# Kernel tuning notes

Hardware: AMD Instinct MI355X
Metric: run time of the kernel (lower is better)

The kernel has to match this reference:

```python
import jax, jax.numpy as jnp
import numpy as np

N_NODES = 100000
N_EDGES = 600000
HID = 128
CH_OUT = 3


def setup_inputs() -> dict:
    key = jax.random.key(0)
    ks = jax.random.split(key, 16)
    s = 0.05  # small init to keep tanh in its linear-ish range
    inp = {
        "x": jax.random.normal(ks[0], (N_NODES, HID), dtype=jnp.float32),
        "pos": jax.random.normal(ks[1], (N_NODES, 3), dtype=jnp.float32),
        "edge_index": jax.random.randint(ks[2], (2, N_EDGES), 0, N_NODES, dtype=jnp.int32),
        "fe_w1": jax.random.normal(ks[3], (2 * HID + 1, HID), dtype=jnp.float32) * s,
        "fe_b1": jnp.zeros((HID,), jnp.float32),
        "fe_w2": jax.random.normal(ks[4], (HID, HID), dtype=jnp.float32) * s,
        "fe_b2": jnp.zeros((HID,), jnp.float32),
        "finf_w": jax.random.normal(ks[5], (HID, 1), dtype=jnp.float32) * s,
        "finf_b": jnp.zeros((1,), jnp.float32),
        "fh_w1": jax.random.normal(ks[6], (2 * HID, HID), dtype=jnp.float32) * s,
        "fh_b1": jnp.zeros((HID,), jnp.float32),
        "fh_w2": jax.random.normal(ks[7], (HID, HID), dtype=jnp.float32) * s,
        "fh_b2": jnp.zeros((HID,), jnp.float32),
        "l1_w": jax.random.normal(ks[8], (HID, HID), dtype=jnp.float32) * s,
        "l1_b": jnp.zeros((HID,), jnp.float32),
        "l2_w": jax.random.normal(ks[9], (HID, HID), dtype=jnp.float32) * s,
        "l2_b": jnp.zeros((HID,), jnp.float32),
        "l3_w": jax.random.normal(ks[10], (HID, HID), dtype=jnp.float32) * s,
        "l3_b": jnp.zeros((HID,), jnp.float32),
        "l4_w": jax.random.normal(ks[11], (HID, HID), dtype=jnp.float32) * s,
        "l4_b": jnp.zeros((HID,), jnp.float32),
        "l5_w": jax.random.normal(ks[12], (HID, CH_OUT), dtype=jnp.float32) * s,
        "l5_b": jnp.zeros((CH_OUT,), jnp.float32),
    }
    return inp


def reference(x, pos, edge_index, fe_w1, fe_b1, fe_w2, fe_b2, finf_w, finf_b,
              fh_w1, fh_b1, fh_w2, fh_b2, l1_w, l1_b, l2_w, l2_b, l3_w, l3_b,
              l4_w, l4_b, l5_w, l5_b):
    e_st, e_end = edge_index[0], edge_index[1]
    # dists = ||(pos_i - pos_j)^2||_2  (norm of the squared difference, as in source)
    d = pos[e_st] - pos[e_end]                                  # [E, 3]
    dists = jnp.linalg.norm(jnp.square(d), axis=1, keepdims=True)  # [E, 1]
    # edge MLP f_e
    tmp = jnp.concatenate([x[e_st], x[e_end], dists], axis=1)   # [E, 2H+1]
    m_ij = jnp.tanh(tmp @ fe_w1 + fe_b1)
    m_ij = jnp.tanh(m_ij @ fe_w2 + fe_b2)                        # [E, H]
    # gating f_inf
    e_ij = jnp.tanh(m_ij @ finf_w + finf_b)                      # [E, 1]
    # scatter-sum to source nodes (index_add on edge_index[0])
    m_i = jax.ops.segment_sum(e_ij * m_ij, e_st, num_segments=x.shape[0])  # [N, H]
    # node update f_h with residual
    h = jnp.concatenate([x, m_i], axis=1)                        # [N, 2H]
    x = x + (jnp.tanh(h @ fh_w1 + fh_b1) @ fh_w2 + fh_b2)
    # dense head (dropout p=0.0 is identity)
    lrelu = lambda v: jax.nn.leaky_relu(v, negative_slope=0.01)
    x = lrelu(x @ l1_w + l1_b)
    x = lrelu(x @ l2_w + l2_b)
    x = lrelu(x @ l3_w + l3_b)
    x = lrelu(x @ l4_w + l4_b)
    return x @ l5_w + l5_b
```

## Files before the change

### kernel.cpp

```cpp
#include <hip/hip_runtime.h>
#include <hip/hip_bf16.h>
#include <math.h>

#define HID 128

typedef unsigned short u16;
typedef __attribute__((ext_vector_type(8))) short bfrag;
typedef __attribute__((ext_vector_type(4))) float f32x4;
typedef __attribute__((ext_vector_type(8))) unsigned short u16x8;
typedef __attribute__((ext_vector_type(4))) unsigned short u16x4;

__device__ __forceinline__ float fast_tanh(float v) {
    float e = __expf(2.0f * v);
    float r = __builtin_amdgcn_rcpf(e + 1.0f);
    return 1.0f - 2.0f * r;
}

__device__ __forceinline__ u16 f2b(float f) {
    __hip_bfloat16 h = __float2bfloat16(f);
    return *(u16*)&h;
}
__device__ __forceinline__ float bits2f(unsigned u) {
    union { unsigned u; float f; } v; v.u = u; return v.f;
}

__global__ void __launch_bounds__(256) prep_combo(
    const float* __restrict__ x, u16* __restrict__ xb,
    const float* __restrict__ w1, const float* __restrict__ fh1,
    const float* __restrict__ w2, const float* __restrict__ fh2,
    const float* __restrict__ l1, const float* __restrict__ l2,
    const float* __restrict__ l3, const float* __restrict__ l4,
    u16* __restrict__ w1t, u16* __restrict__ fh1t,
    u16* __restrict__ w2t, u16* __restrict__ fh2t,
    u16* __restrict__ l1t, u16* __restrict__ l2t,
    u16* __restrict__ l3t, u16* __restrict__ l4t,
    const int* __restrict__ est, int* __restrict__ cnt, int E, int nxb)
{
    int b = blockIdx.x, t = threadIdx.x;
    if (b < nxb) {
        int i = b * 256 + t;
        const float4 v0 = *(const float4*)(x + (size_t)i * 8);
        const float4 v1 = *(const float4*)(x + (size_t)i * 8 + 4);
        u16x8 o = { f2b(v0.x), f2b(v0.y), f2b(v0.z), f2b(v0.w),
                    f2b(v1.x), f2b(v1.y), f2b(v1.z), f2b(v1.w) };
        *(u16x8*)(xb + (size_t)i * 8) = o;
        return;
    }
    b -= nxb;
    if (b < 640) {
        const float* src; u16* dst; int K;
        if (b < 256) {
            K = 256;
            if (b < 128) { src = w1;  dst = w1t; }
            else         { src = fh1; dst = fh1t; b -= 128; }
        } else {
            K = 128;
            int s = (b - 256) >> 6; b = (b - 256) & 63;
            switch (s) {
                case 0:  src = w2;  dst = w2t;  break;
                case 1:  src = fh2; dst = fh2t; break;
                case 2:  src = l1;  dst = l1t;  break;
                case 3:  src = l2;  dst = l2t;  break;
                case 4:  src = l3;  dst = l3t;  break;
                default: src = l4;  dst = l4t;  break;
            }
        }
        int idx = b * 256 + t;
        int k = idx >> 7, n = idx & 127;
        dst[(size_t)n * K + k] = f2b(src[(size_t)k * 128 + n]);
        return;
    }
    b -= 640;
    int e = b * 256 + t;
    if (e < E) atomicAdd(&cnt[est[e]], 1);
}

__global__ void __launch_bounds__(256) scan1(const int* __restrict__ cnt,
                                             int* __restrict__ scanout,
                                             int* __restrict__ partial, int N) {
    __shared__ int s[256];
    int t = threadIdx.x, b = blockIdx.x, i = b * 256 + t;
    int v = (i < N) ? cnt[i] : 0;
    s[t] = v; __syncthreads();
#pragma unroll
    for (int d = 1; d < 256; d <<= 1) {
        int add = (t >= d) ? s[t - d] : 0;
        __syncthreads();
        s[t] += add;
        __syncthreads();
    }
    if (i < N) scanout[i] = s[t] - v;
    if (t == 255) partial[b] = s[255];
}

__global__ void __launch_bounds__(512) scan2(int* __restrict__ partial, int NB) {
    __shared__ int s[512];
    int t = threadIdx.x;
    int v = (t < NB) ? partial[t] : 0;
    s[t] = v; __syncthreads();
#pragma unroll
    for (int d = 1; d < 512; d <<= 1) {
        int add = (t >= d) ? s[t - d] : 0;
        __syncthreads();
        s[t] += add;
        __syncthreads();
    }
    if (t < NB) partial[t] = s[t] - v;
}

__global__ void __launch_bounds__(256) scan3(const int* __restrict__ scanout,
                                             const int* __restrict__ partial,
                                             int* __restrict__ offs,
                                             int* __restrict__ cur, int N, int E) {
    int t = threadIdx.x, b = blockIdx.x, i = b * 256 + t;
    if (i < N) { int o = scanout[i] + partial[b]; offs[i] = o; cur[i] = o; }
    if (i == 0) offs[N] = E;
}

__global__ void __launch_bounds__(256) reorder_kernel(const int* __restrict__ est,
                                                      const int* __restrict__ eend,
                                                      int* __restrict__ cur,
                                                      int* __restrict__ est_s,
                                                      int* __restrict__ eend_s, int E) {
    int e = blockIdx.x * 256 + threadIdx.x;
    if (e < E) {
        int s = est[e];
        int p = atomicAdd(&cur[s], 1);
        est_s[p]  = s;
        eend_s[p] = eend[e];
    }
}

template<int KD>
__device__ __forceinline__ void gemm_k(const u16* sbuf, const u16* __restrict__ wt,
                                       int w, int l16, int l4g, f32x4 (&acc)[2][2]) {
    const int RS = KD * 2;
#pragma unroll
    for (int k0 = 0; k0 < KD; k0 += 32) {
        const int kb = k0 * 2 + l4g * 16;
        bfrag a0 = *(const bfrag*)((const char*)sbuf +
                    (unsigned)((l16 * RS + kb) ^ ((l16 & 7) << 4)));
        bfrag a1 = *(const bfrag*)((const char*)sbuf +
                    (unsigned)(((16 + l16) * RS + kb) ^ ((l16 & 7) << 4)));
        bfrag b0 = *(const bfrag*)((const char*)wt + (size_t)(32 * w + l16) * RS + kb);
        bfrag b1 = *(const bfrag*)((const char*)wt + (size_t)(32 * w + 16 + l16) * RS + kb);
        acc[0][0] = __builtin_amdgcn_mfma_f32_16x16x32_bf16(a0, b0, acc[0][0], 0, 0, 0);
        acc[0][1] = __builtin_amdgcn_mfma_f32_16x16x32_bf16(a0, b1, acc[0][1], 0, 0, 0);
        acc[1][0] = __builtin_amdgcn_mfma_f32_16x16x32_bf16(a1, b0, acc[1][0], 0, 0, 0);
        acc[1][1] = __builtin_amdgcn_mfma_f32_16x16x32_bf16(a1, b1, acc[1][1], 0, 0, 0);
    }
}

template<int KD>
__device__ __forceinline__ void gemm_sw(const u16* act, const u16* __restrict__ wt,
                                        int w, int l16, int l4g, f32x4 (&acc)[2][2]) {
    const int RS = KD * 2;
#pragma unroll
    for (int k0 = 0; k0 < KD; k0 += 32) {
        const int kb = k0 * 2 + l4g * 16;
        bfrag wa0 = *(const bfrag*)((const char*)wt + (size_t)(32 * w + l16) * RS + kb);
        bfrag wa1 = *(const bfrag*)((const char*)wt + (size_t)(32 * w + 16 + l16) * RS + kb);
        bfrag be0 = *(const bfrag*)((const char*)act +
                    (unsigned)((l16 * RS + kb) ^ ((l16 & 7) << 4)));
        bfrag be1 = *(const bfrag*)((const char*)act +
                    (unsigned)(((16 + l16) * RS + kb) ^ ((l16 & 7) << 4)));
        acc[0][0] = __builtin_amdgcn_mfma_f32_16x16x32_bf16(wa0, be0, acc[0][0], 0, 0, 0);
        acc[0][1] = __builtin_amdgcn_mfma_f32_16x16x32_bf16(wa0, be1, acc[0][1], 0, 0, 0);
        acc[1][0] = __builtin_amdgcn_mfma_f32_16x16x32_bf16(wa1, be0, acc[1][0], 0, 0, 0);
        acc[1][1] = __builtin_amdgcn_mfma_f32_16x16x32_bf16(wa1, be1, acc[1][1], 0, 0, 0);
    }
}

__global__ void __launch_bounds__(256, 2)
egc_edge_csr(const u16* __restrict__ xb, const float* __restrict__ pos,
             const int* __restrict__ est_s, const int* __restrict__ eend_s,
             const u16* __restrict__ w1t, const float* __restrict__ w1last,
             const float* __restrict__ b1, const u16* __restrict__ w2t,
             const float* __restrict__ b2, const float* __restrict__ fw,
             const float* __restrict__ fb, u16* __restrict__ g,
             float* __restrict__ ev, int n_tiles)
{
    __shared__ __attribute__((aligned(16))) u16 a_sh[2][32 * 256];
    __shared__ __attribute__((aligned(16))) u16 m1_sh[32 * 128];
    __shared__ float red[32][17];
    __shared__ float dist_l[2][32];

    const int t = threadIdx.x, lane = t & 63, w = t >> 6;
    const int l16 = lane & 15, l4g = lane >> 4;
    const unsigned swz = (unsigned)((l16 & 7) << 4);

    bfrag wa10[8], wa11[8], w2f0[4], w2f1[4];
#pragma unroll
    for (int i = 0; i < 8; ++i) {
        int kb = i * 64 + l4g * 16;
        wa10[i] = *(const bfrag*)((const char*)w1t + (size_t)(32 * w + l16) * 512 + kb);
        wa11[i] = *(const bfrag*)((const char*)w1t + (size_t)(32 * w + 16 + l16) * 512 + kb);
    }
#pragma unroll
    for (int i = 0; i < 4; ++i) {
        int kb = i * 64 + l4g * 16;
        w2f0[i] = *(const bfrag*)((const char*)w2t + (size_t)(32 * w + l16) * 256 + kb);
        w2f1[i] = *(const bfrag*)((const char*)w2t + (size_t)(32 * w + 16 + l16) * 256 + kb);
    }
    float w1l_r[2][4], b1_r[2][4], b2_r[2][4], fw_r[2][4];
#pragma unroll
    for (int mi = 0; mi < 2; ++mi)
#pragma unroll
        for (int rg = 0; rg < 4; ++rg) {
            int n = 32 * w + 16 * mi + l4g * 4 + rg;
            w1l_r[mi][rg] = w1last[n];
            b1_r[mi][rg]  = b1[n];
            b2_r[mi][rg]  = b2[n];
            fw_r[mi][rg]  = fw[n];
        }
    const float fbv = fb[0];

    float4 sv0, sv1, sv2, sv3;
    float pax = 0, pay = 0, paz = 0, pbx = 0, pby = 0, pbz = 0;

#define EDGE_ISSUE(TILE) do {                                                  \
        int e0_ = (TILE) * 32;                                                 \
        { int f_ = t;       int e_ = f_ >> 5, q_ = f_ & 31; int ge_ = e0_ + e_;\
          int nd_ = (q_ < 16) ? est_s[ge_] : eend_s[ge_];                      \
          sv0 = *(const float4*)(xb + (size_t)nd_ * 128 + (q_ & 15) * 8); }    \
        { int f_ = t + 256; int e_ = f_ >> 5, q_ = f_ & 31; int ge_ = e0_ + e_;\
          int nd_ = (q_ < 16) ? est_s[ge_] : eend_s[ge_];                      \
          sv1 = *(const float4*)(xb + (size_t)nd_ * 128 + (q_ & 15) * 8); }    \
        { int f_ = t + 512; int e_ = f_ >> 5, q_ = f_ & 31; int ge_ = e0_ + e_;\
          int nd_ = (q_ < 16) ? est_s[ge_] : eend_s[ge_];                      \
          sv2 = *(const float4*)(xb + (size_t)nd_ * 128 + (q_ & 15) * 8); }    \
        { int f_ = t + 768; int e_ = f_ >> 5, q_ = f_ & 31; int ge_ = e0_ + e_;\
          int nd_ = (q_ < 16) ? est_s[ge_] : eend_s[ge_];                      \
          sv3 = *(const float4*)(xb + (size_t)nd_ * 128 + (q_ & 15) * 8); }    \
        if (t < 32) {                                                          \
            int ge_ = e0_ + t;                                                 \
            int a_ = est_s[ge_], b_ = eend_s[ge_];                             \
            pax = pos[a_ * 3]; pay = pos[a_ * 3 + 1]; paz = pos[a_ * 3 + 2];   \
            pbx = pos[b_ * 3]; pby = pos[b_ * 3 + 1]; pbz = pos[b_ * 3 + 2];   \
        }                                                                      \
    } while (0)

#define EDGE_COMMIT(BUF) do {                                                  \
        { int f_ = t;       int e_ = f_ >> 5, q_ = f_ & 31;                    \
          unsigned by_ = (unsigned)(e_ * 512 + q_ * 16) ^ (unsigned)((e_ & 7) << 4); \
          *(float4*)((char*)a_sh[BUF] + by_) = sv0; }                          \
        { int f_ = t + 256; int e_ = f_ >> 5, q_ = f_ & 31;                    \
          unsigned by_ = (unsigned)(e_ * 512 + q_ * 16) ^ (unsigned)((e_ & 7) << 4); \
          *(float4*)((char*)a_sh[BUF] + by_) = sv1; }                          \
        { int f_ = t + 512; int e_ = f_ >> 5, q_ = f_ & 31;                    \
          unsigned by_ = (unsigned)(e_ * 512 + q_ * 16) ^ (unsigned)((e_ & 7) << 4); \
          *(float4*)((char*)a_sh[BUF] + by_) = sv2; }                          \
        { int f_ = t + 768; int e_ = f_ >> 5, q_ = f_ & 31;                    \
          unsigned by_ = (unsigned)(e_ * 512 + q_ * 16) ^ (unsigned)((e_ & 7) << 4); \
          *(float4*)((char*)a_sh[BUF] + by_) = sv3; }                          \
        if (t < 32) {                                                          \
            float dx_ = pax - pbx, dy_ = pay - pby, dz_ = paz - pbz;           \
            dx_ *= dx_; dy_ *= dy_; dz_ *= dz_;                                \
            dist_l[BUF][t] = sqrtf(dx_ * dx_ + dy_ * dy_ + dz_ * dz_);         \
        }                                                                      \
    } while (0)

    int tile = blockIdx.x;
    EDGE_ISSUE(tile);
    int buf = 0;

    if (tile < n_tiles)
    while (true) {
        EDGE_COMMIT(buf);
        __syncthreads();
        int next = tile + gridDim.x;
        if (next < n_tiles) EDGE_ISSUE(next);
        const int e0 = tile * 32;

        {
            f32x4 acc[2][2] = {};
#pragma unroll
            for (int i = 0; i < 8; ++i) {
                int kb = i * 64 + l4g * 16;
                bfrag be0 = *(const bfrag*)((const char*)a_sh[buf] +
                            ((unsigned)(l16 * 512 + kb) ^ swz));
                bfrag be1 = *(const bfrag*)((const char*)a_sh[buf] +
                            ((unsigned)((16 + l16) * 512 + kb) ^ swz));
                acc[0][0] = __builtin_amdgcn_mfma_f32_16x16x32_bf16(wa10[i], be0, acc[0][0], 0, 0, 0);
                acc[0][1] = __builtin_amdgcn_mfma_f32_16x16x32_bf16(wa10[i], be1, acc[0][1], 0, 0, 0);
                acc[1][0] = __builtin_amdgcn_mfma_f32_16x16x32_bf16(wa11[i], be0, acc[1][0], 0, 0, 0);
                acc[1][1] = __builtin_amdgcn_mfma_f32_16x16x32_bf16(wa11[i], be1, acc[1][1], 0, 0, 0);
            }
            float de0 = dist_l[buf][l16];
            float de1 = dist_l[buf][16 + l16];
#pragma unroll
            for (int mi = 0; mi < 2; ++mi)
#pragma unroll
                for (int ni = 0; ni < 2; ++ni) {
                    float de = ni ? de1 : de0;
                    u16x4 pk;
#pragma unroll
                    for (int rg = 0; rg < 4; ++rg) {
                        float v = fast_tanh(acc[mi][ni][rg] + de * w1l_r[mi][rg] + b1_r[mi][rg]);
                        pk[rg] = f2b(v);
                    }
                    unsigned byte = ((unsigned)((16 * ni + l16) * 256 +
                                     (32 * w + 16 * mi + l4g * 4) * 2)) ^ swz;
                    *(u16x4*)((char*)m1_sh + byte) = pk;
                }
        }
        __syncthreads();

        {
            f32x4 acc[2][2] = {};
#pragma unroll
            for (int i = 0; i < 4; ++i) {
                int kb = i * 64 + l4g * 16;
                bfrag me0 = *(const bfrag*)((const char*)m1_sh +
                            ((unsigned)(l16 * 256 + kb) ^ swz));
                bfrag me1 = *(const bfrag*)((const char*)m1_sh +
                            ((unsigned)((16 + l16) * 256 + kb) ^ swz));
                acc[0][0] = __builtin_amdgcn_mfma_f32_16x16x32_bf16(w2f0[i], me0, acc[0][0], 0, 0, 0);
                acc[0][1] = __builtin_amdgcn_mfma_f32_16x16x32_bf16(w2f0[i], me1, acc[0][1], 0, 0, 0);
                acc[1][0] = __builtin_amdgcn_mfma_f32_16x16x32_bf16(w2f1[i], me0, acc[1][0], 0, 0, 0);
                acc[1][1] = __builtin_amdgcn_mfma_f32_16x16x32_bf16(w2f1[i], me1, acc[1][1], 0, 0, 0);
            }
            float part0 = 0.0f, part1 = 0.0f;
#pragma unroll
            for (int mi = 0; mi < 2; ++mi)
#pragma unroll
                for (int ni = 0; ni < 2; ++ni) {
                    u16x4 pk;
                    float ps = 0.0f;
#pragma unroll
                    for (int rg = 0; rg < 4; ++rg) {
                        float v = fast_tanh(acc[mi][ni][rg] + b2_r[mi][rg]);
                        ps += v * fw_r[mi][rg];
                        pk[rg] = f2b(v);
                    }
                    if (ni) part1 += ps; else part0 += ps;
                    int dstrow = e0 + 16 * ni + l16;
                    *(u16x4*)(g + (size_t)dstrow * 128 + (32 * w + 16 * mi + l4g * 4)) = pk;
                }
            red[l16][w * 4 + l4g]      = part0;
            red[16 + l16][w * 4 + l4g] = part1;
        }
        __syncthreads();

        if (t < 32) {
            float s = 0.0f;
#pragma unroll
            for (int j = 0; j < 16; ++j) s += red[t][j];
            ev[e0 + t] = fast_tanh(s + fbv);
        }

        tile = next; buf ^= 1;
        if (tile >= n_tiles) break;
    }
#undef EDGE_ISSUE
#undef EDGE_COMMIT
}

__global__ void __launch_bounds__(256, 8)
gather_seq(const u16* __restrict__ g, const float* __restrict__ ev,
           const int* __restrict__ offs, u16* __restrict__ m_i)
{
    const int lane = threadIdx.x & 63;
    const int half = lane >> 5;
    const int l32  = lane & 31;
    const int n = blockIdx.x * 4 + (threadIdx.x >> 6);
    const int beg = offs[n], end = offs[n + 1];
    float a0 = 0.0f, a1 = 0.0f, a2 = 0.0f, a3 = 0.0f;
    for (int e = beg + half; e < end; e += 2) {
        uint2 v = *(const uint2*)(g + (size_t)e * 128 + l32 * 4);
        float ee = ev[e];
        a0 += ee * bits2f(v.x << 16);
        a1 += ee * bits2f(v.x & 0xFFFF0000u);
        a2 += ee * bits2f(v.y << 16);
        a3 += ee * bits2f(v.y & 0xFFFF0000u);
    }
    a0 += __shfl_xor(a0, 32);
    a1 += __shfl_xor(a1, 32);
    a2 += __shfl_xor(a2, 32);
    a3 += __shfl_xor(a3, 32);
    if (half == 0) {
        uint2 o;
        o.x = (unsigned)f2b(a0) | ((unsigned)f2b(a1) << 16);
        o.y = (unsigned)f2b(a2) | ((unsigned)f2b(a3) << 16);
        *(uint2*)(m_i + (size_t)n * 128 + l32 * 4) = o;
    }
}

__global__ void __launch_bounds__(256, 3)
egc_edge_mfma(const u16* __restrict__ xb, const float* __restrict__ pos,
              const int* __restrict__ est, const int* __restrict__ eend,
              const u16* __restrict__ w1t, const float* __restrict__ w1last,
              const float* __restrict__ b1, const u16* __restrict__ w2t,
              const float* __restrict__ b2, const float* __restrict__ fw,
              const float* __restrict__ fb, float* __restrict__ m_i)
{
    __shared__ __attribute__((aligned(16))) u16 a_sh[32 * 256];
    __shared__ __attribute__((aligned(16))) u16 m1_sh[32 * 128];
    __shared__ float m2_sh[32][132];
    __shared__ float dist_l[32];
    __shared__ float ev_l[32];
    __shared__ int   st_l[32];

    const int t = threadIdx.x;
    const int e0 = blockIdx.x * 32;
    const int lane = t & 63;
    const int w = t >> 6;
    const int l16 = lane & 15, l4g = lane >> 4;

#pragma unroll
    for (int i = 0; i < 4; ++i) {
        int f = t + 256 * i;
        int e = f >> 5, q = f & 31;
        int ge = e0 + e;
        int node = (q < 16) ? est[ge] : eend[ge];
        float4 v = *(const float4*)(xb + (size_t)node * 128 + (q & 15) * 8);
        unsigned byte = (unsigned)(e * 512 + q * 16) ^ (unsigned)((e & 7) << 4);
        *(float4*)((char*)a_sh + byte) = v;
    }
    if (t < 32) {
        int ge = e0 + t;
        int a = est[ge], b = eend[ge];
        st_l[t] = a;
        float dx = pos[a * 3 + 0] - pos[b * 3 + 0];
        float dy = pos[a * 3 + 1] - pos[b * 3 + 1];
        float dz = pos[a * 3 + 2] - pos[b * 3 + 2];
        dx *= dx; dy *= dy; dz *= dz;
        dist_l[t] = sqrtf(dx * dx + dy * dy + dz * dz);
    }
    __syncthreads();

    {
        f32x4 acc[2][2] = {};
        gemm_k<256>(a_sh, w1t, w, l16, l4g, acc);
#pragma unroll
        for (int mi = 0; mi < 2; ++mi)
#pragma unroll
            for (int ni = 0; ni < 2; ++ni) {
                const int col = 32 * w + 16 * ni + l16;
                const float wl = w1last[col], bb = b1[col];
#pragma unroll
                for (int rg = 0; rg < 4; ++rg) {
                    const int row = 16 * mi + l4g * 4 + rg;
                    float v = fast_tanh(acc[mi][ni][rg] + dist_l[row] * wl + bb);
                    unsigned byte = (unsigned)((row * 256 + col * 2) ^ ((row & 7) << 4));
                    *(u16*)((char*)m1_sh + byte) = f2b(v);
                }
            }
    }
    __syncthreads();

    {
        f32x4 acc[2][2] = {};
        gemm_k<128>(m1_sh, w2t, w, l16, l4g, acc);
#pragma unroll
        for (int mi = 0; mi < 2; ++mi)
#pragma unroll
            for (int ni = 0; ni < 2; ++ni) {
                const int col = 32 * w + 16 * ni + l16;
                const float bb = b2[col];
#pragma unroll
                for (int rg = 0; rg < 4; ++rg) {
                    const int row = 16 * mi + l4g * 4 + rg;
                    m2_sh[row][col] = fast_tanh(acc[mi][ni][rg] + bb);
                }
            }
    }
    __syncthreads();

    if (t < 128) {
        int e = t >> 2, p = t & 3;
        float s = 0.0f;
#pragma unroll
        for (int k = 0; k < 32; ++k) s += m2_sh[e][p * 32 + k] * fw[p * 32 + k];
        s += __shfl_xor(s, 1);
        s += __shfl_xor(s, 2);
        if (p == 0) ev_l[e] = fast_tanh(s + fb[0]);
    }
    __syncthreads();

    {
        int e = t >> 3, l8 = t & 7;
        float ev = ev_l[e];
        size_t base = (size_t)st_l[e] * HID + l8;
#pragma unroll
        for (int i = 0; i < 16; ++i)
            unsafeAtomicAdd(m_i + base + 8 * i, ev * m2_sh[e][l8 + 8 * i]);
    }
}

#define NODE_LAYER_SW(SRC, KD, WT, BIAS, DST, ACT)                             \
    {                                                                          \
        f32x4 acc[2][2] = {};                                                  \
        gemm_sw<KD>(SRC, WT, w, l16, l4g, acc);                                \
        float bbr[2][4];                                                       \
        _Pragma("unroll")                                                      \
        for (int mi = 0; mi < 2; ++mi)                                         \
            _Pragma("unroll")                                                  \
            for (int rg = 0; rg < 4; ++rg)                                     \
                bbr[mi][rg] = (BIAS)[32 * w + 16 * mi + l4g * 4 + rg];         \
        _Pragma("unroll")                                                      \
        for (int mi = 0; mi < 2; ++mi)                                         \
            _Pragma("unroll")                                                  \
            for (int ni = 0; ni < 2; ++ni) {                                   \
                const int node = 16 * ni + l16;                                \
                const int ch = 32 * w + 16 * mi + l4g * 4;                     \
                u16x4 pk;                                                      \
                _Pragma("unroll")                                              \
                for (int rg = 0; rg < 4; ++rg) {                               \
                    float v = acc[mi][ni][rg] + bbr[mi][rg];                   \
                    ACT;                                                       \
                    pk[rg] = f2b(v);                                           \
                }                                                              \
                unsigned byte = ((unsigned)(node * 256 + ch * 2)) ^ swz;       \
                *(u16x4*)((char*)(DST) + byte) = pk;                           \
            }                                                                  \
    }

template<int MODE>
__global__ void __launch_bounds__(256, 3)
egc_node_mfma(const u16* __restrict__ xb, const float* __restrict__ xf,
              const void* __restrict__ m_i,
              const u16* __restrict__ fh1t, const float* __restrict__ hb1,
              const u16* __restrict__ fh2t, const float* __restrict__ hb2,
              const u16* __restrict__ l1t, const float* __restrict__ l1b,
              const u16* __restrict__ l2t, const float* __restrict__ l2b,
              const u16* __restrict__ l3t, const float* __restrict__ l3b,
              const u16* __restrict__ l4t, const float* __restrict__ l4b,
              const float* __restrict__ l5w, const float* __restrict__ l5b,
              float* __restrict__ out)
{
    __shared__ __attribute__((aligned(16))) u16 a_sh[32 * 256];
    __shared__ __attribute__((aligned(16))) u16 bA[32 * 128];
    __shared__ __attribute__((aligned(16))) u16 bB[32 * 128];
    __shared__ float red[32][3][17];

    const int t = threadIdx.x;
    const int n0 = blockIdx.x * 32;
    const int lane = t & 63;
    const int w = t >> 6;
    const int l16 = lane & 15, l4g = lane >> 4;
    const unsigned swz = (unsigned)((l16 & 7) << 4);

#pragma unroll
    for (int i = 0; i < 2; ++i) {
        int f = t + 256 * i;
        int n = f >> 4, q = f & 15;
        float4 v = *(const float4*)(xb + (size_t)(n0 + n) * 128 + q * 8);
        unsigned byte = (unsigned)((n * 512 + q * 16) ^ ((n & 7) << 4));
        *(float4*)((char*)a_sh + byte) = v;
    }
    if (MODE == 0) {
#pragma unroll
        for (int i = 0; i < 2; ++i) {
            int f = t + 256 * i;
            int n = f >> 4, q = f & 15;
            float4 v = *(const float4*)((const u16*)m_i + (size_t)(n0 + n) * 128 + q * 8);
            unsigned byte = (unsigned)((n * 512 + 256 + q * 16) ^ ((n & 7) << 4));
            *(float4*)((char*)a_sh + byte) = v;
        }
    } else {
#pragma unroll
        for (int i = 0; i < 2; ++i) {
            int f = t + 256 * i;
            int n = f >> 4, q = f & 15;
            const float* src = (const float*)m_i + (size_t)(n0 + n) * 128 + q * 8;
            float4 v0 = *(const float4*)(src);
            float4 v1 = *(const float4*)(src + 4);
            u16x8 o = { f2b(v0.x), f2b(v0.y), f2b(v0.z), f2b(v0.w),
                        f2b(v1.x), f2b(v1.y), f2b(v1.z), f2b(v1.w) };
            unsigned byte = (unsigned)((n * 512 + 256 + q * 16) ^ ((n & 7) << 4));
            *(u16x8*)((char*)a_sh + byte) = o;
        }
    }
    __syncthreads();

    NODE_LAYER_SW(a_sh, 256, fh1t, hb1, bA, { v = fast_tanh(v); })
    __syncthreads();

    {
        f32x4 acc[2][2] = {};
        gemm_sw<128>(bA, fh2t, w, l16, l4g, acc);
        float bbr[2][4];
#pragma unroll
        for (int mi = 0; mi < 2; ++mi)
#pragma unroll
            for (int rg = 0; rg < 4; ++rg)
                bbr[mi][rg] = hb2[32 * w + 16 * mi + l4g * 4 + rg];
#pragma unroll
        for (int mi = 0; mi < 2; ++mi)
#pragma unroll
            for (int ni = 0; ni < 2; ++ni) {
                const int node = 16 * ni + l16;
                const int ch = 32 * w + 16 * mi + l4g * 4;
                float4 xr = *(const float4*)(xf + (size_t)(n0 + node) * 128 + ch);
                u16x4 pk;
                pk[0] = f2b(acc[mi][ni][0] + bbr[mi][0] + xr.x);
                pk[1] = f2b(acc[mi][ni][1] + bbr[mi][1] + xr.y);
                pk[2] = f2b(acc[mi][ni][2] + bbr[mi][2] + xr.z);
                pk[3] = f2b(acc[mi][ni][3] + bbr[mi][3] + xr.w);
                unsigned byte = ((unsigned)(node * 256 + ch * 2)) ^ swz;
                *(u16x4*)((char*)bB + byte) = pk;
            }
    }
    __syncthreads();

    NODE_LAYER_SW(bB, 128, l1t, l1b, bA, { v = v > 0.0f ? v : 0.01f * v; })
    __syncthreads();
    NODE_LAYER_SW(bA, 128, l2t, l2b, bB, { v = v > 0.0f ? v : 0.01f * v; })
    __syncthreads();
    NODE_LAYER_SW(bB, 128, l3t, l3b, bA, { v = v > 0.0f ? v : 0.01f * v; })
    __syncthreads();

    {
        f32x4 acc[2][2] = {};
        gemm_sw<128>(bA, l4t, w, l16, l4g, acc);
        float bbr[2][4], w5[2][4][3];
#pragma unroll
        for (int mi = 0; mi < 2; ++mi)
#pragma unroll
            for (int rg = 0; rg < 4; ++rg) {
                int ch = 32 * w + 16 * mi + l4g * 4 + rg;
                bbr[mi][rg] = l4b[ch];
#pragma unroll
                for (int cc = 0; cc < 3; ++cc) w5[mi][rg][cc] = l5w[ch * 3 + cc];
            }
#pragma unroll
        for (int ni = 0; ni < 2; ++ni) {
            float p0 = 0.0f, p1 = 0.0f, p2 = 0.0f;
#pragma unroll
            for (int mi = 0; mi < 2; ++mi)
#pragma unroll
                for (int rg = 0; rg < 4; ++rg) {
                    float v = acc[mi][ni][rg] + bbr[mi][rg];
                    v = v > 0.0f ? v : 0.01f * v;
                    p0 += v * w5[mi][rg][0];
                    p1 += v * w5[mi][rg][1];
                    p2 += v * w5[mi][rg][2];
                }
            const int n = 16 * ni + l16, j = w * 4 + l4g;
            red[n][0][j] = p0;
            red[n][1][j] = p1;
            red[n][2][j] = p2;
        }
    }
    __syncthreads();

    if (t < 96) {
        int n = t / 3, cc = t % 3;
        float s = l5b[cc];
#pragma unroll
        for (int j = 0; j < 16; ++j) s += red[n][cc][j];
        out[(size_t)(n0 + n) * 3 + cc] = s;
    }
}

extern "C" void kernel_launch(void* const* d_in, const int* in_sizes, int n_in,
                              void* d_out, int out_size, void* d_ws, size_t ws_size,
                              hipStream_t stream)
{
    const float* x      = (const float*)d_in[0];
    const float* pos    = (const float*)d_in[1];
    const int*   eidx   = (const int*)d_in[2];
    const float* fe_w1  = (const float*)d_in[3];
    const float* fe_b1  = (const float*)d_in[4];
    const float* fe_w2  = (const float*)d_in[5];
    const float* fe_b2  = (const float*)d_in[6];
    const float* finf_w = (const float*)d_in[7];
    const float* finf_b = (const float*)d_in[8];
    const float* fh_w1  = (const float*)d_in[9];
    const float* fh_b1  = (const float*)d_in[10];
    const float* fh_w2  = (const float*)d_in[11];
    const float* fh_b2  = (const float*)d_in[12];
    const float* l1w    = (const float*)d_in[13];
    const float* l1b    = (const float*)d_in[14];
    const float* l2w    = (const float*)d_in[15];
    const float* l2b    = (const float*)d_in[16];
    const float* l3w    = (const float*)d_in[17];
    const float* l3b    = (const float*)d_in[18];
    const float* l4w    = (const float*)d_in[19];
    const float* l4b    = (const float*)d_in[20];
    const float* l5w    = (const float*)d_in[21];
    const float* l5b    = (const float*)d_in[22];
    float* out = (float*)d_out;

    const int n_edges = in_sizes[2] / 2;
    const int n_nodes = in_sizes[0] / HID;
    const int nsb     = (n_nodes + 255) / 256;
    const int n_tiles = n_edges / 32;
    const int nxb     = (n_nodes * HID) / (256 * 8);
    const int nhb     = (n_edges + 255) / 256;

    char* ws = (char*)d_ws;
    const bool use_csr = (ws_size >= 208800000ULL);

    if (use_csr) {
        u16* g     = (u16*)(ws + 0);
        u16* xb    = (u16*)(ws + 153600000);
        u16* m_i   = (u16*)(ws + 179200000);
        int* est_s  = (int*)(ws + 179200000);
        int* eend_s = (int*)(ws + 181600000);
        u16* w1t  = (u16*)(ws + 204800000);
        u16* w2t  = (u16*)(ws + 204865536);
        u16* fh1t = (u16*)(ws + 204898304);
        u16* fh2t = (u16*)(ws + 204963840);
        u16* l1t  = (u16*)(ws + 204996608);
        u16* l2t  = (u16*)(ws + 205029376);
        u16* l3t  = (u16*)(ws + 205062144);
        u16* l4t  = (u16*)(ws + 205094912);
        int* cnt  = (int*)(ws + 205127680);
        int* offs = (int*)(ws + 205527680);
        int* cur  = (int*)(ws + 205927696);
        float* ev = (float*)(ws + 206327696);
        int* part = (int*)(ws + 208727696);

        (void)hipMemsetAsync(cnt, 0, (size_t)n_nodes * sizeof(int), stream);
        prep_combo<<<dim3(nxb + 640 + nhb), dim3(256), 0, stream>>>(
            x, xb, fe_w1, fh_w1, fe_w2, fh_w2, l1w, l2w, l3w, l4w,
            w1t, fh1t, w2t, fh2t, l1t, l2t, l3t, l4t, eidx, cnt, n_edges, nxb);

        scan1<<<dim3(nsb), dim3(256), 0, stream>>>(cnt, cnt, part, n_nodes);
        scan2<<<dim3(1), dim3(512), 0, stream>>>(part, nsb);
        scan3<<<dim3(nsb), dim3(256), 0, stream>>>(cnt, part, offs, cur, n_nodes, n_edges);
        reorder_kernel<<<dim3(nhb), dim3(256), 0, stream>>>(
            eidx, eidx + n_edges, cur, est_s, eend_s, n_edges);

        egc_edge_csr<<<dim3(512), dim3(256), 0, stream>>>(
            xb, pos, est_s, eend_s, w1t, fe_w1 + (size_t)256 * HID, fe_b1,
            w2t, fe_b2, finf_w, finf_b, g, ev, n_tiles);

        gather_seq<<<dim3(n_nodes / 4), dim3(256), 0, stream>>>(g, ev, offs, m_i);

        egc_node_mfma<0><<<dim3(n_nodes / 32), dim3(256), 0, stream>>>(
            xb, x, m_i, fh1t, fh_b1, fh2t, fh_b2, l1t, l1b, l2t, l2b,
            l3t, l3b, l4t, l4b, l5w, l5b, out);
    } else {
        float* m_i = (float*)(ws + 0);
        u16* xb    = (u16*)(ws + 51200000);
        u16* w1t   = (u16*)(ws + 76800000);
        u16* w2t   = (u16*)(ws + 76865536);
        u16* fh1t  = (u16*)(ws + 76898304);
        u16* fh2t  = (u16*)(ws + 76963840);
        u16* l1t   = (u16*)(ws + 76996608);
        u16* l2t   = (u16*)(ws + 77029376);
        u16* l3t   = (u16*)(ws + 77062144);
        u16* l4t   = (u16*)(ws + 77094912);

        (void)hipMemsetAsync(m_i, 0, (size_t)n_nodes * HID * sizeof(float), stream);
        prep_combo<<<dim3(nxb + 640), dim3(256), 0, stream>>>(
            x, xb, fe_w1, fh_w1, fe_w2, fh_w2, l1w, l2w, l3w, l4w,
            w1t, fh1t, w2t, fh2t, l1t, l2t, l3t, l4t, eidx, (int*)d_ws, 0, nxb);

        egc_edge_mfma<<<dim3(n_edges / 32), dim3(256), 0, stream>>>(
            xb, pos, eidx, eidx + n_edges, w1t, fe_w1 + (size_t)256 * HID, fe_b1,
            w2t, fe_b2, finf_w, finf_b, m_i);

        egc_node_mfma<1><<<dim3(n_nodes / 32), dim3(256), 0, stream>>>(
            xb, x, m_i, fh1t, fh_b1, fh2t, fh_b2, l1t, l1b, l2t, l2b,
            l3t, l3b, l4t, l4b, l5w, l5b, out);
    }
}
```

Measured before the change: 358.5 us.

## Defer edge gate reduction to next iteration, unroll gather loop, raise node occupancy

The edge kernel drops one __syncthreads per tile by finishing the gate reduction for the previous tile after the next tile's barrier, with a final flush after the loop. The gather kernel is unrolled by two with independent accumulators, so more loads are in flight per thread. The node kernel's launch bounds go from 3 to 4 blocks per SM to raise occupancy, which may squeeze registers and cause spills. The deferred reduction relies on red[] not being overwritten before it is read, which the barrier ordering appears to guarantee.

```diff
diff --git a/kernel.cpp b/kernel.cpp
--- a/kernel.cpp
+++ b/kernel.cpp
@@ -263,11 +263,18 @@
     int tile = blockIdx.x;
     EDGE_ISSUE(tile);
     int buf = 0;
+    int prev_e0 = -1;
 
     if (tile < n_tiles)
     while (true) {
         EDGE_COMMIT(buf);
         __syncthreads();
+        if (prev_e0 >= 0 && t < 32) {
+            float s = 0.0f;
+#pragma unroll
+            for (int j = 0; j < 16; ++j) s += red[t][j];
+            ev[prev_e0 + t] = fast_tanh(s + fbv);
+        }
         int next = tile + gridDim.x;
         if (next < n_tiles) EDGE_ISSUE(next);
         const int e0 = tile * 32;
@@ -340,17 +347,17 @@
             red[l16][w * 4 + l4g]      = part0;
             red[16 + l16][w * 4 + l4g] = part1;
         }
-        __syncthreads();
-
-        if (t < 32) {
-            float s = 0.0f;
-#pragma unroll
-            for (int j = 0; j < 16; ++j) s += red[t][j];
-            ev[e0 + t] = fast_tanh(s + fbv);
-        }
-
+
+        prev_e0 = e0;
         tile = next; buf ^= 1;
         if (tile >= n_tiles) break;
+    }
+    __syncthreads();
+    if (prev_e0 >= 0 && t < 32) {
+        float s = 0.0f;
+#pragma unroll
+        for (int j = 0; j < 16; ++j) s += red[t][j];
+        ev[prev_e0 + t] = fast_tanh(s + fbv);
     }
 #undef EDGE_ISSUE
 #undef EDGE_COMMIT
@@ -366,14 +373,30 @@
     const int n = blockIdx.x * 4 + (threadIdx.x >> 6);
     const int beg = offs[n], end = offs[n + 1];
     float a0 = 0.0f, a1 = 0.0f, a2 = 0.0f, a3 = 0.0f;
-    for (int e = beg + half; e < end; e += 2) {
-        uint2 v = *(const uint2*)(g + (size_t)e * 128 + l32 * 4);
-        float ee = ev[e];
-        a0 += ee * bits2f(v.x << 16);
-        a1 += ee * bits2f(v.x & 0xFFFF0000u);
-        a2 += ee * bits2f(v.y << 16);
-        a3 += ee * bits2f(v.y & 0xFFFF0000u);
-    }
+    float b0 = 0.0f, b1 = 0.0f, b2 = 0.0f, b3 = 0.0f;
+    int e = beg + half;
+    for (; e + 3 < end; e += 4) {
+        uint2 v0 = *(const uint2*)(g + (size_t)e * 128 + l32 * 4);
+        uint2 v1 = *(const uint2*)(g + (size_t)(e + 2) * 128 + l32 * 4);
+        float e0 = ev[e], e1 = ev[e + 2];
+        a0 += e0 * bits2f(v0.x << 16);
+        a1 += e0 * bits2f(v0.x & 0xFFFF0000u);
+        a2 += e0 * bits2f(v0.y << 16);
+        a3 += e0 * bits2f(v0.y & 0xFFFF0000u);
+        b0 += e1 * bits2f(v1.x << 16);
+        b1 += e1 * bits2f(v1.x & 0xFFFF0000u);
+        b2 += e1 * bits2f(v1.y << 16);
+        b3 += e1 * bits2f(v1.y & 0xFFFF0000u);
+    }
+    for (; e < end; e += 2) {
+        uint2 v0 = *(const uint2*)(g + (size_t)e * 128 + l32 * 4);
+        float e0 = ev[e];
+        a0 += e0 * bits2f(v0.x << 16);
+        a1 += e0 * bits2f(v0.x & 0xFFFF0000u);
+        a2 += e0 * bits2f(v0.y << 16);
+        a3 += e0 * bits2f(v0.y & 0xFFFF0000u);
+    }
+    a0 += b0; a1 += b1; a2 += b2; a3 += b3;
     a0 += __shfl_xor(a0, 32);
     a1 += __shfl_xor(a1, 32);
     a2 += __shfl_xor(a2, 32);
@@ -517,7 +540,7 @@
     }
 
 template<int MODE>
-__global__ void __launch_bounds__(256, 3)
+__global__ void __launch_bounds__(256, 4)
 egc_node_mfma(const u16* __restrict__ xb, const float* __restrict__ xf,
               const void* __restrict__ m_i,
               const u16* __restrict__ fh1t, const float* __restrict__ hb1,
```

Result: faster. 344.2 us (-4.0%).
